# Optimization experiments

Measured on AMD Instinct MI355X. Metric: run time of the kernel, lower is better.

## Reference

```python
import jax, jax.numpy as jnp
import numpy as np

N_NODES = 100000
N_GRAPHS = 512
NEG_SLOPE = 0.2
EPS = 1e-16


def gat_conv(x, W, a_src, a_dst, bias, src, dst, heads, out_ch, concat):
    # x: [N, Fin]; W: [Fin, heads*out_ch]; a_src/a_dst: [heads, out_ch]
    N = x.shape[0]
    h = (x @ W).reshape(N, heads, out_ch)                      # [N,H,C]
    alpha_src = jnp.einsum('nhc,hc->nh', h, a_src)             # [N,H]
    alpha_dst = jnp.einsum('nhc,hc->nh', h, a_dst)             # [N,H]
    e = alpha_src[src] + alpha_dst[dst]                        # [E,H]
    e = jnp.where(e > 0, e, NEG_SLOPE * e)                     # leaky relu
    # segment softmax over incoming edges per destination node
    m = jax.ops.segment_max(e, dst, num_segments=N)            # [N,H]
    m = jnp.where(jnp.isfinite(m), m, 0.0)
    ee = jnp.exp(e - m[dst])
    denom = jax.ops.segment_sum(ee, dst, num_segments=N)       # [N,H]
    alpha = ee / (denom[dst] + EPS)                            # [E,H]
    msg = h[src] * alpha[:, :, None]                           # [E,H,C]
    out = jax.ops.segment_sum(msg, dst, num_segments=N)        # [N,H,C]
    if concat:
        out = out.reshape(N, heads * out_ch)
    else:
        out = out.mean(axis=1)
    return out + bias


def setup_inputs() -> dict:
    key = jax.random.key(0)
    ks = jax.random.split(key, 12)
    x = jax.random.normal(ks[0], (N_NODES, 128), dtype=jnp.float32)
    edge_index = jax.random.randint(ks[1], (2, 1600000), 0, N_NODES, dtype=jnp.int64)
    batch = jnp.sort(jax.random.randint(ks[2], (N_NODES,), 0, N_GRAPHS, dtype=jnp.int64))
    s = 0.1
    W1 = jax.random.normal(ks[3], (128, 64), dtype=jnp.float32) * s
    a_src1 = jax.random.normal(ks[4], (8, 8), dtype=jnp.float32) * s
    a_dst1 = jax.random.normal(ks[5], (8, 8), dtype=jnp.float32) * s
    b1 = jnp.zeros((64,), dtype=jnp.float32)
    W2 = jax.random.normal(ks[6], (64, 10), dtype=jnp.float32) * s
    a_src2 = jax.random.normal(ks[7], (1, 10), dtype=jnp.float32) * s
    a_dst2 = jax.random.normal(ks[8], (1, 10), dtype=jnp.float32) * s
    b2 = jnp.zeros((10,), dtype=jnp.float32)
    return {"x": x, "edge_index": edge_index, "batch": batch,
            "W1": W1, "a_src1": a_src1, "a_dst1": a_dst1, "b1": b1,
            "W2": W2, "a_src2": a_src2, "a_dst2": a_dst2, "b2": b2}


def reference(x, edge_index, batch, W1, a_src1, a_dst1, b1, W2, a_src2, a_dst2, b2):
    N = x.shape[0]
    # PyG GATConv default add_self_loops=True
    loops = jnp.arange(N, dtype=edge_index.dtype)
    src = jnp.concatenate([edge_index[0], loops])
    dst = jnp.concatenate([edge_index[1], loops])
    # eval mode: dropout layers are identity
    h = gat_conv(x, W1, a_src1, a_dst1, b1, src, dst, heads=8, out_ch=8, concat=True)
    h = jax.nn.elu(h)
    h = gat_conv(h, W2, a_src2, a_dst2, b2, src, dst, heads=1, out_ch=10, concat=False)
    # global mean pool over graphs
    sums = jax.ops.segment_sum(h, batch, num_segments=N_GRAPHS)        # [G,10]
    cnts = jax.ops.segment_sum(jnp.ones((N, 1), h.dtype), batch, num_segments=N_GRAPHS)
    pooled = sums / jnp.maximum(cnts, 1.0)
    return jax.nn.log_softmax(pooled, axis=1)
```

## Files before the change

kernel.cpp:

```cpp
#include <hip/hip_runtime.h>
#include <math.h>

#define L2E 1.44269504088896f
#define LRELU(v) fmaxf((v), 0.2f * (v))

__device__ __forceinline__ float fexp2(float v) { return __builtin_amdgcn_exp2f(v); }
__device__ __forceinline__ float felu(float r) {
    return r > 0.f ? r : fexp2(r * L2E) - 1.f;
}

__device__ __forceinline__ unsigned short f2bf(float f) {
    unsigned u = __float_as_uint(f);
    u += 0x7FFFu + ((u >> 16) & 1u);
    return (unsigned short)(u >> 16);
}
__device__ __forceinline__ float bf2f(unsigned short b) {
    return __uint_as_float((unsigned)b << 16);
}

typedef __attribute__((ext_vector_type(8))) short bf16x8;
typedef __attribute__((ext_vector_type(4))) float f32x4;

#define UPD8(mm, dd, Aa, Ab, ev, U)                                       \
    {                                                                     \
        float mn_ = fmaxf(mm, ev);                                        \
        float sc_ = fexp2(mm - mn_);                                      \
        float w_  = fexp2(ev - mn_);                                      \
        dd = dd * sc_ + w_;                                               \
        Aa.x = Aa.x * sc_ + w_ * __uint_as_float((U).x << 16);            \
        Aa.y = Aa.y * sc_ + w_ * __uint_as_float((U).x & 0xffff0000u);    \
        Aa.z = Aa.z * sc_ + w_ * __uint_as_float((U).y << 16);            \
        Aa.w = Aa.w * sc_ + w_ * __uint_as_float((U).y & 0xffff0000u);    \
        Ab.x = Ab.x * sc_ + w_ * __uint_as_float((U).z << 16);            \
        Ab.y = Ab.y * sc_ + w_ * __uint_as_float((U).z & 0xffff0000u);    \
        Ab.z = Ab.z * sc_ + w_ * __uint_as_float((U).w << 16);            \
        Ab.w = Ab.w * sc_ + w_ * __uint_as_float((U).w & 0xffff0000u);    \
        mm = mn_;                                                         \
    }
#define UPD1(mm, dd, aa, ev, hv)           \
    {                                      \
        float mn_ = fmaxf(mm, ev);         \
        float sc_ = fexp2(mm - mn_);       \
        float w_  = fexp2(ev - mn_);       \
        dd = dd * sc_ + w_;                \
        aa = aa * sc_ + w_ * (hv);         \
        mm = mn_;                          \
    }

#define CH 4096

__global__ __launch_bounds__(256) void k_gemm1_mfma(
        const float* __restrict__ x, const float* __restrict__ W,
        unsigned short* __restrict__ h1b, int N, int ntiles) {
    int tid = threadIdx.x;
    int w = tid >> 6, l = tid & 63;
    int c0 = w * 16;
    int lr = l & 15;
    int lg = l >> 4;

    bf16x8 bfr[4];
#pragma unroll
    for (int kk = 0; kk < 4; ++kk)
#pragma unroll
        for (int j = 0; j < 8; ++j)
            bfr[kk][j] = (short)f2bf(W[(size_t)(kk * 32 + lg * 8 + j) * 64 + c0 + lr]);

    for (int t = blockIdx.x; t < ntiles; t += gridDim.x) {
        int n0 = t * 16;
        int n = n0 + lr;
        const float4* xr = (const float4*)(x + (size_t)(n < N ? n : 0) * 128);
        f32x4 acc = {0.f, 0.f, 0.f, 0.f};
#pragma unroll
        for (int kk = 0; kk < 4; ++kk) {
            float4 u0 = xr[kk * 8 + lg * 2];
            float4 u1 = xr[kk * 8 + lg * 2 + 1];
            bf16x8 afr;
            afr[0] = (short)f2bf(u0.x); afr[1] = (short)f2bf(u0.y);
            afr[2] = (short)f2bf(u0.z); afr[3] = (short)f2bf(u0.w);
            afr[4] = (short)f2bf(u1.x); afr[5] = (short)f2bf(u1.y);
            afr[6] = (short)f2bf(u1.z); afr[7] = (short)f2bf(u1.w);
            acc = __builtin_amdgcn_mfma_f32_16x16x32_bf16(afr, bfr[kk], acc, 0, 0, 0);
        }
#pragma unroll
        for (int r = 0; r < 4; ++r) {
            int nn = n0 + lg * 4 + r;
            if (nn < N) h1b[(size_t)nn * 64 + c0 + lr] = f2bf(acc[r]);
        }
    }
}

__global__ void k_alpha(const unsigned short* __restrict__ h1b,
                        const float* __restrict__ a_src, const float* __restrict__ a_dst,
                        unsigned short* __restrict__ asrcb, float* __restrict__ adst, int N) {
    int t = blockIdx.x * 256 + threadIdx.x;
    if (t >= N * 8) return;
    int n = t >> 3, h = t & 7;
    uint4 hw = *(const uint4*)&h1b[(size_t)n * 64 + h * 8];
    const unsigned short* hu = (const unsigned short*)&hw;
    const float* as = a_src + h * 8;
    const float* ad = a_dst + h * 8;
    float s = 0.f, d = 0.f;
#pragma unroll
    for (int c = 0; c < 8; ++c) {
        float hv = bf2f(hu[c]);
        s = fmaf(hv, as[c], s);
        d = fmaf(hv, ad[c], d);
    }
    asrcb[t] = f2bf(s * L2E);
    adst[t] = d * L2E;
}


__global__ __launch_bounds__(256) void k_bhist(const int* __restrict__ dstE,
                                               const int* __restrict__ batch,
                                               int E, int NB, int G, int* __restrict__ bh) {
    __shared__ int lh[512];
    int tid = threadIdx.x, b = blockIdx.x;
    lh[tid] = 0; lh[tid + 256] = 0;
    __syncthreads();
#pragma unroll
    for (int i = 0; i < CH / 1024; ++i) {
        int eb = b * CH + (i * 256 + tid) * 4;
        if (eb + 3 < E) {
            int4 dv = *(const int4*)(dstE + eb);
            int g0 = batch[dv.x], g1 = batch[dv.y], g2 = batch[dv.z], g3 = batch[dv.w];
            atomicAdd(&lh[g0], 1); atomicAdd(&lh[g1], 1);
            atomicAdd(&lh[g2], 1); atomicAdd(&lh[g3], 1);
        } else {
#pragma unroll
            for (int k = 0; k < 4; ++k)
                if (eb + k < E) atomicAdd(&lh[batch[dstE[eb + k]]], 1);
        }
    }
    __syncthreads();
    if (tid < G)       bh[(size_t)tid * NB + b] = lh[tid];
    if (tid + 256 < G) bh[(size_t)(tid + 256) * NB + b] = lh[tid + 256];
}

__global__ __launch_bounds__(512) void k_mscan(const int* __restrict__ bh, int NB,
                                               int* __restrict__ pstart, int* __restrict__ total) {
    __shared__ int buf[512];
    int bin = blockIdx.x, t = threadIdx.x;
    int v = (t < NB) ? bh[(size_t)bin * NB + t] : 0;
    buf[t] = v;
    __syncthreads();
    for (int off = 1; off < 512; off <<= 1) {
        int u = (t >= off) ? buf[t - off] : 0;
        __syncthreads();
        buf[t] += u;
        __syncthreads();
    }
    if (t < NB) pstart[(size_t)bin * NB + t] = buf[t] - v;
    if (t == 511) total[bin] = buf[511];
}

__global__ __launch_bounds__(1024) void k_scan_top(const int* __restrict__ total, int nb,
                                                   int* __restrict__ boff,
                                                   const int* __restrict__ batch, int N,
                                                   int* __restrict__ nstart) {
    __shared__ int buf[1024];
    int t = threadIdx.x;
    int v = (t < nb) ? total[t] : 0;
    buf[t] = v;
    __syncthreads();
    for (int off = 1; off < 1024; off <<= 1) {
        int u = (t >= off) ? buf[t - off] : 0;
        __syncthreads();
        buf[t] += u;
        __syncthreads();
    }
    if (t < nb) {
        boff[t] = buf[t] - v;
        int lo = 0, hi = N;
        while (lo < hi) { int mid = (lo + hi) >> 1; if (batch[mid] < t) lo = mid + 1; else hi = mid; }
        nstart[t] = lo;
    }
}

__global__ __launch_bounds__(256) void k_bscatter(const int* __restrict__ srcE,
                                                  const int* __restrict__ dstE,
                                                  const int* __restrict__ batch,
                                                  const int* __restrict__ boff,
                                                  const int* __restrict__ pstart,
                                                  const int* __restrict__ nstart,
                                                  int E, int NB, int G, int* __restrict__ pairs) {
    __shared__ int lstart[512];
    __shared__ int lc[512];
    __shared__ int lns[512];
    int tid = threadIdx.x, b = blockIdx.x;
#pragma unroll
    for (int j = tid; j < 512; j += 256) {
        lstart[j] = (j < G) ? boff[j] + pstart[(size_t)j * NB + b] : 0;
        lns[j] = (j < G) ? nstart[j] : 0;
        lc[j] = 0;
    }
    __syncthreads();
#pragma unroll
    for (int i = 0; i < CH / 1024; ++i) {
        int eb = b * CH + (i * 256 + tid) * 4;
        if (eb + 3 < E) {
            int4 sv = *(const int4*)(srcE + eb);
            int4 dv = *(const int4*)(dstE + eb);
            int g0 = batch[dv.x], g1 = batch[dv.y], g2 = batch[dv.z], g3 = batch[dv.w];
            int p0 = atomicAdd(&lc[g0], 1);
            int p1 = atomicAdd(&lc[g1], 1);
            int p2 = atomicAdd(&lc[g2], 1);
            int p3 = atomicAdd(&lc[g3], 1);
            pairs[lstart[g0] + p0] = sv.x | ((dv.x - lns[g0]) << 17);
            pairs[lstart[g1] + p1] = sv.y | ((dv.y - lns[g1]) << 17);
            pairs[lstart[g2] + p2] = sv.z | ((dv.z - lns[g2]) << 17);
            pairs[lstart[g3] + p3] = sv.w | ((dv.w - lns[g3]) << 17);
        } else {
#pragma unroll
            for (int k = 0; k < 4; ++k)
                if (eb + k < E) {
                    int s = srcE[eb + k], d = dstE[eb + k];
                    int bin = batch[d];
                    int old = atomicAdd(&lc[bin], 1);
                    pairs[lstart[bin] + old] = s | ((d - lns[bin]) << 17);
                }
        }
    }
}

__global__ __launch_bounds__(512) void k_csr_local(const int* __restrict__ pairs,
                                                   const int* __restrict__ boff,
                                                   const int* __restrict__ batch,
                                                   int E, int N, int G,
                                                   int* __restrict__ cnt, int* __restrict__ excl,
                                                   int* __restrict__ srcs) {
    __shared__ int lcnt[512];
    __shared__ int buf[512];
    __shared__ int lcur[512];
    int g = blockIdx.x, t = threadIdx.x;
    int lo = 0, hi = N;
    while (lo < hi) { int mid = (lo + hi) >> 1; if (batch[mid] < g) lo = mid + 1; else hi = mid; }
    int ns = lo;
    hi = N;
    while (lo < hi) { int mid = (lo + hi) >> 1; if (batch[mid] < g + 1) lo = mid + 1; else hi = mid; }
    int ne = lo;
    int lnodes = ne - ns;
    int es = boff[g];
    int ee = (g + 1 < G) ? boff[g + 1] : E;

    lcnt[t] = 0;
    __syncthreads();
    for (int e = es + t; e < ee; e += 512) atomicAdd(&lcnt[pairs[e] >> 17], 1);
    __syncthreads();
    int v = lcnt[t];
    buf[t] = v;
    __syncthreads();
    for (int off = 1; off < 512; off <<= 1) {
        int u = (t >= off) ? buf[t - off] : 0;
        __syncthreads();
        buf[t] += u;
        __syncthreads();
    }
    int lex = buf[t] - v;
    lcur[t] = lex;
    if (t < lnodes) {
        cnt[ns + t] = v;
        excl[ns + t] = es + lex;
    }
    __syncthreads();
    for (int e = es + t; e < ee; e += 512) {
        int pv = pairs[e];
        int pos = atomicAdd(&lcur[pv >> 17], 1);
        srcs[es + pos] = pv & 0x1FFFF;
    }
}

__global__ void k_gather1(const int* __restrict__ srcs, const int* __restrict__ excl,
                          const int* __restrict__ cnt,
                          const unsigned short* __restrict__ asrcb, const float* __restrict__ adst1,
                          const unsigned short* __restrict__ h1b,
                          const float* __restrict__ b1, const float* __restrict__ W2,
                          const float* __restrict__ a_src2, const float* __restrict__ a_dst2,
                          unsigned short* __restrict__ h2b, unsigned short* __restrict__ asrc2b,
                          float* __restrict__ adst2, int N) {
    int tid = blockIdx.x * 256 + threadIdx.x;
    int wave = tid >> 6;
    int lane = threadIdx.x & 63;
    int q = lane >> 3;
    int l = lane & 7;
    int wid = wave * 8 + q;
    if (wid >= N) return;
    int c0 = l * 8;

    int beg = excl[wid];
    int cw  = cnt[wid];
    const int* sp = srcs + beg;
    float adh = adst1[wid * 8 + l];

    uint4 us = *(const uint4*)&h1b[(size_t)wid * 64 + c0];
    float4 A0a, A0b;
    A0a.x = __uint_as_float(us.x << 16); A0a.y = __uint_as_float(us.x & 0xffff0000u);
    A0a.z = __uint_as_float(us.y << 16); A0a.w = __uint_as_float(us.y & 0xffff0000u);
    A0b.x = __uint_as_float(us.z << 16); A0b.y = __uint_as_float(us.z & 0xffff0000u);
    A0b.z = __uint_as_float(us.w << 16); A0b.w = __uint_as_float(us.w & 0xffff0000u);
    float m0 = LRELU(bf2f(asrcb[wid * 8 + l]) + adh), d0 = 1.f;
    float4 Z = {0.f, 0.f, 0.f, 0.f};
    float4 A1a = Z, A1b = Z, A2a = Z, A2b = Z, A3a = Z, A3b = Z;
    float m1 = -INFINITY, d1 = 0.f;
    float m2 = -INFINITY, d2 = 0.f;
    float m3 = -INFINITY, d3 = 0.f;

    int i = 0;
    for (; i + 4 <= cw; i += 4) {
        int s0 = sp[i], s1 = sp[i + 1], s2 = sp[i + 2], s3 = sp[i + 3];
        float e0 = LRELU(bf2f(asrcb[s0 * 8 + l]) + adh);
        float e1 = LRELU(bf2f(asrcb[s1 * 8 + l]) + adh);
        float e2 = LRELU(bf2f(asrcb[s2 * 8 + l]) + adh);
        float e3 = LRELU(bf2f(asrcb[s3 * 8 + l]) + adh);
        uint4 u0 = *(const uint4*)&h1b[(size_t)s0 * 64 + c0];
        uint4 u1 = *(const uint4*)&h1b[(size_t)s1 * 64 + c0];
        uint4 u2 = *(const uint4*)&h1b[(size_t)s2 * 64 + c0];
        uint4 u3 = *(const uint4*)&h1b[(size_t)s3 * 64 + c0];
        UPD8(m0, d0, A0a, A0b, e0, u0);
        UPD8(m1, d1, A1a, A1b, e1, u1);
        UPD8(m2, d2, A2a, A2b, e2, u2);
        UPD8(m3, d3, A3a, A3b, e3, u3);
    }
    for (; i < cw; ++i) {
        int s = sp[i];
        float ev = LRELU(bf2f(asrcb[s * 8 + l]) + adh);
        uint4 uv = *(const uint4*)&h1b[(size_t)s * 64 + c0];
        UPD8(m0, d0, A0a, A0b, ev, uv);
    }
    float mM = fmaxf(fmaxf(m0, m1), fmaxf(m2, m3));
    float w0 = fexp2(m0 - mM), w1 = fexp2(m1 - mM);
    float w2 = fexp2(m2 - mM), w3 = fexp2(m3 - mM);
    float den = d0 * w0 + d1 * w1 + d2 * w2 + d3 * w3;
    float inv = 1.f / (den + 1e-16f);
    float rv[8];
    rv[0] = (A0a.x * w0 + A1a.x * w1 + A2a.x * w2 + A3a.x * w3) * inv;
    rv[1] = (A0a.y * w0 + A1a.y * w1 + A2a.y * w2 + A3a.y * w3) * inv;
    rv[2] = (A0a.z * w0 + A1a.z * w1 + A2a.z * w2 + A3a.z * w3) * inv;
    rv[3] = (A0a.w * w0 + A1a.w * w1 + A2a.w * w2 + A3a.w * w3) * inv;
    rv[4] = (A0b.x * w0 + A1b.x * w1 + A2b.x * w2 + A3b.x * w3) * inv;
    rv[5] = (A0b.y * w0 + A1b.y * w1 + A2b.y * w2 + A3b.y * w3) * inv;
    rv[6] = (A0b.z * w0 + A1b.z * w1 + A2b.z * w2 + A3b.z * w3) * inv;
    rv[7] = (A0b.w * w0 + A1b.w * w1 + A2b.w * w2 + A3b.w * w3) * inv;

    float accj[10];
#pragma unroll
    for (int j = 0; j < 10; ++j) accj[j] = 0.f;
#pragma unroll
    for (int t = 0; t < 8; ++t) {
        float r = felu(rv[t] + b1[c0 + t]);
        const float* wr = W2 + (c0 + t) * 10;
#pragma unroll
        for (int j = 0; j < 10; ++j) accj[j] = fmaf(r, wr[j], accj[j]);
    }
#pragma unroll
    for (int mask = 1; mask <= 4; mask <<= 1)
#pragma unroll
        for (int j = 0; j < 10; ++j) accj[j] += __shfl_xor(accj[j], mask);

    if (l == 0) {
        float s = 0.f, d = 0.f;
        unsigned pw[5];
#pragma unroll
        for (int j = 0; j < 10; j += 2) {
            s = fmaf(accj[j], a_src2[j], s);     d = fmaf(accj[j], a_dst2[j], d);
            s = fmaf(accj[j+1], a_src2[j+1], s); d = fmaf(accj[j+1], a_dst2[j+1], d);
            pw[j >> 1] = (unsigned)f2bf(accj[j]) | ((unsigned)f2bf(accj[j+1]) << 16);
        }
        unsigned* hw = (unsigned*)&h2b[(size_t)wid * 10];
#pragma unroll
        for (int j = 0; j < 5; ++j) hw[j] = pw[j];
        asrc2b[wid] = f2bf(s * L2E);
        adst2[wid] = d * L2E;
    }
}

__global__ void k_gather2(const int* __restrict__ srcs, const int* __restrict__ excl,
                          const int* __restrict__ cnt,
                          const unsigned short* __restrict__ asrc2b, const float* __restrict__ adst2,
                          const unsigned short* __restrict__ h2b, float* __restrict__ agg2, int N) {
    int tid = blockIdx.x * 256 + threadIdx.x;
    int wave = tid >> 6;
    int lane = threadIdx.x & 63;
    int q = lane >> 4;
    int l = lane & 15;
    int wid = wave * 4 + q;
    if (wid >= N) return;

    int beg = excl[wid];
    int cw  = cnt[wid];
    const int* sp = srcs + beg;
    float adn = adst2[wid];
    bool ld = l < 10;

    float m0 = LRELU(bf2f(asrc2b[wid]) + adn), d0 = 1.f;
    float a0 = ld ? bf2f(h2b[(size_t)wid * 10 + l]) : 0.f;
    float m1 = -INFINITY, d1 = 0.f, a1 = 0.f;
    float m2 = -INFINITY, d2 = 0.f, a2 = 0.f;
    float m3 = -INFINITY, d3 = 0.f, a3 = 0.f;

    int i = 0;
    for (; i + 4 <= cw; i += 4) {
        int s0 = sp[i], s1 = sp[i + 1], s2 = sp[i + 2], s3 = sp[i + 3];
        float e0 = LRELU(bf2f(asrc2b[s0]) + adn);
        float e1 = LRELU(bf2f(asrc2b[s1]) + adn);
        float e2 = LRELU(bf2f(asrc2b[s2]) + adn);
        float e3 = LRELU(bf2f(asrc2b[s3]) + adn);
        float g0 = ld ? bf2f(h2b[(size_t)s0 * 10 + l]) : 0.f;
        float g1 = ld ? bf2f(h2b[(size_t)s1 * 10 + l]) : 0.f;
        float g2 = ld ? bf2f(h2b[(size_t)s2 * 10 + l]) : 0.f;
        float g3 = ld ? bf2f(h2b[(size_t)s3 * 10 + l]) : 0.f;
        UPD1(m0, d0, a0, e0, g0);
        UPD1(m1, d1, a1, e1, g1);
        UPD1(m2, d2, a2, e2, g2);
        UPD1(m3, d3, a3, e3, g3);
    }
    for (; i < cw; ++i) {
        int s = sp[i];
        float ev = LRELU(bf2f(asrc2b[s]) + adn);
        float gv = ld ? bf2f(h2b[(size_t)s * 10 + l]) : 0.f;
        UPD1(m0, d0, a0, ev, gv);
    }
    float mM = fmaxf(fmaxf(m0, m1), fmaxf(m2, m3));
    float w0 = fexp2(m0 - mM), w1 = fexp2(m1 - mM);
    float w2 = fexp2(m2 - mM), w3 = fexp2(m3 - mM);
    float den = d0 * w0 + d1 * w1 + d2 * w2 + d3 * w3;
    float acc = a0 * w0 + a1 * w1 + a2 * w2 + a3 * w3;
    if (ld) agg2[(size_t)wid * 10 + l] = acc / (den + 1e-16f);
}

__global__ void k_pool_final(const float* __restrict__ agg2, const float* __restrict__ b2,
                             const int* __restrict__ batch, float* __restrict__ out,
                             int N, int G) {
    int g = blockIdx.x;
    int lo = 0, hi = N;
    while (lo < hi) { int mid = (lo + hi) >> 1; if (batch[mid] < g) lo = mid + 1; else hi = mid; }
    int s = lo;
    lo = s; hi = N;
    while (lo < hi) { int mid = (lo + hi) >> 1; if (batch[mid] < g + 1) lo = mid + 1; else hi = mid; }
    int e = lo;
    int tid = threadIdx.x;
    float acc[10];
#pragma unroll
    for (int j = 0; j < 10; ++j) acc[j] = 0.f;
    for (int n = s + tid; n < e; n += 256) {
        const float* r = agg2 + (size_t)n * 10;
#pragma unroll
        for (int j = 0; j < 10; ++j) acc[j] += r[j];
    }
    __shared__ float red[256 * 10];
#pragma unroll
    for (int j = 0; j < 10; ++j) red[tid * 10 + j] = acc[j];
    __syncthreads();
    for (int st = 128; st > 0; st >>= 1) {
        if (tid < st)
#pragma unroll
            for (int j = 0; j < 10; ++j) red[tid * 10 + j] += red[(tid + st) * 10 + j];
        __syncthreads();
    }
    if (tid == 0) {
        int c = e - s;
        float v[10], m = -1e30f;
#pragma unroll
        for (int j = 0; j < 10; ++j) {
            v[j] = (c > 0) ? red[j] / (float)c + b2[j] : 0.f;
            m = fmaxf(m, v[j]);
        }
        float ssum = 0.f;
#pragma unroll
        for (int j = 0; j < 10; ++j) ssum += expf(v[j] - m);
        float ls = logf(ssum);
#pragma unroll
        for (int j = 0; j < 10; ++j) out[(size_t)g * 10 + j] = v[j] - m - ls;
    }
}

extern "C" void kernel_launch(void* const* d_in, const int* in_sizes, int n_in,
                              void* d_out, int out_size, void* d_ws, size_t ws_size,
                              hipStream_t stream) {
    const float* x     = (const float*)d_in[0];
    const int*   ei    = (const int*)d_in[1];
    const int*   batch = (const int*)d_in[2];
    const float* W1    = (const float*)d_in[3];
    const float* as1w  = (const float*)d_in[4];
    const float* ad1w  = (const float*)d_in[5];
    const float* b1    = (const float*)d_in[6];
    const float* W2    = (const float*)d_in[7];
    const float* as2w  = (const float*)d_in[8];
    const float* ad2w  = (const float*)d_in[9];
    const float* b2    = (const float*)d_in[10];

    const int N  = in_sizes[0] / 128;
    const int E  = in_sizes[1] / 2;
    const int G  = out_size / 10;
    const int* srcE = ei;
    const int* dstE = ei + E;

    auto cdiv = [](long long a, long long b) { return (int)((a + b - 1) / b); };
    const int NB = cdiv(E, CH);

    size_t Nz = (size_t)N;
    unsigned short* h1b = (unsigned short*)d_ws;
    float* agg2  = (float*)d_ws;
    unsigned short* asrc1b = h1b + Nz * 64;
    float* adst1 = (float*)(asrc1b + Nz * 8);
    unsigned short* h2b = (unsigned short*)(adst1 + Nz * 8);
    unsigned short* asrc2b = h2b + Nz * 10;
    float* adst2 = (float*)(asrc2b + Nz + (Nz & 1));
    int* pairsA  = (int*)(adst2 + Nz);
    int* cntA    = pairsA + (size_t)E;
    int* exclA   = cntA + Nz;
    int* srcsA   = exclA + Nz;
    int* bhA     = srcsA + E;
    int* pstartA = bhA + (size_t)512 * NB;
    int* totalA  = pstartA + (size_t)512 * NB;
    int* boffA   = totalA + 512;
    int* nstartA = boffA + 512;

    const int B = 256;

    int ntiles = cdiv(N, 16);
    int gB = ntiles < 2048 ? ntiles : 2048;
    k_gemm1_mfma<<<gB, B, 0, stream>>>(x, W1, h1b, N, ntiles);
    k_alpha<<<cdiv((long long)N * 8, B), B, 0, stream>>>(h1b, as1w, ad1w, asrc1b, adst1, N);

    k_bhist<<<NB, B, 0, stream>>>(dstE, batch, E, NB, G, bhA);
    k_mscan<<<512, 512, 0, stream>>>(bhA, NB, pstartA, totalA);
    k_scan_top<<<1, 1024, 0, stream>>>(totalA, G, boffA, batch, N, nstartA);
    k_bscatter<<<NB, B, 0, stream>>>(srcE, dstE, batch, boffA, pstartA, nstartA, E, NB, G, pairsA);
    k_csr_local<<<G, 512, 0, stream>>>(pairsA, boffA, batch, E, N, G, cntA, exclA, srcsA);

    k_gather1<<<cdiv(N, 32), B, 0, stream>>>(srcsA, exclA, cntA, asrc1b, adst1, h1b,
                                             b1, W2, as2w, ad2w, h2b, asrc2b, adst2, N);

    k_gather2<<<cdiv(N, 16), B, 0, stream>>>(srcsA, exclA, cntA, asrc2b, adst2, h2b, agg2, N);

    k_pool_final<<<G, B, 0, stream>>>(agg2, b2, batch, (float*)d_out, N, G);
}
```

Before: 190.7 us.

## Fuse attention-logit computation into GEMM epilogue and fold top scan into mscan

```diff
diff --git a/kernel.cpp b/kernel.cpp
--- a/kernel.cpp
+++ b/kernel.cpp
@@ -51,7 +51,9 @@
 
 __global__ __launch_bounds__(256) void k_gemm1_mfma(
         const float* __restrict__ x, const float* __restrict__ W,
-        unsigned short* __restrict__ h1b, int N, int ntiles) {
+        const float* __restrict__ a_src, const float* __restrict__ a_dst,
+        unsigned short* __restrict__ h1b, unsigned short* __restrict__ asrcb,
+        float* __restrict__ adst1, int N, int ntiles) {
     int tid = threadIdx.x;
     int w = tid >> 6, l = tid & 63;
     int c0 = w * 16;
@@ -64,6 +66,9 @@
 #pragma unroll
         for (int j = 0; j < 8; ++j)
             bfr[kk][j] = (short)f2bf(W[(size_t)(kk * 32 + lg * 8 + j) * 64 + c0 + lr]);
+
+    float asv = a_src[c0 + lr];
+    float adv = a_dst[c0 + lr];
 
     for (int t = blockIdx.x; t < ntiles; t += gridDim.x) {
         int n0 = t * 16;
@@ -86,36 +91,38 @@
             int nn = n0 + lg * 4 + r;
             if (nn < N) h1b[(size_t)nn * 64 + c0 + lr] = f2bf(acc[r]);
         }
-    }
-}
-
-__global__ void k_alpha(const unsigned short* __restrict__ h1b,
-                        const float* __restrict__ a_src, const float* __restrict__ a_dst,
-                        unsigned short* __restrict__ asrcb, float* __restrict__ adst, int N) {
-    int t = blockIdx.x * 256 + threadIdx.x;
-    if (t >= N * 8) return;
-    int n = t >> 3, h = t & 7;
-    uint4 hw = *(const uint4*)&h1b[(size_t)n * 64 + h * 8];
-    const unsigned short* hu = (const unsigned short*)&hw;
-    const float* as = a_src + h * 8;
-    const float* ad = a_dst + h * 8;
-    float s = 0.f, d = 0.f;
-#pragma unroll
-    for (int c = 0; c < 8; ++c) {
-        float hv = bf2f(hu[c]);
-        s = fmaf(hv, as[c], s);
-        d = fmaf(hv, ad[c], d);
-    }
-    asrcb[t] = f2bf(s * L2E);
-    adst[t] = d * L2E;
+        float ps[4], pd[4];
+#pragma unroll
+        for (int r = 0; r < 4; ++r) { ps[r] = acc[r] * asv; pd[r] = acc[r] * adv; }
+#pragma unroll
+        for (int mask = 1; mask <= 4; mask <<= 1)
+#pragma unroll
+            for (int r = 0; r < 4; ++r) {
+                ps[r] += __shfl_xor(ps[r], mask);
+                pd[r] += __shfl_xor(pd[r], mask);
+            }
+        if ((lr & 7) == 0) {
+            int h = (c0 + lr) >> 3;
+#pragma unroll
+            for (int r = 0; r < 4; ++r) {
+                int nn = n0 + lg * 4 + r;
+                if (nn < N) {
+                    asrcb[nn * 8 + h] = f2bf(ps[r] * L2E);
+                    adst1[nn * 8 + h] = pd[r] * L2E;
+                }
+            }
+        }
+    }
 }
 
 
 __global__ __launch_bounds__(256) void k_bhist(const int* __restrict__ dstE,
                                                const int* __restrict__ batch,
-                                               int E, int NB, int G, int* __restrict__ bh) {
+                                               int E, int NB, int G, int* __restrict__ bh,
+                                               int* __restrict__ done) {
     __shared__ int lh[512];
     int tid = threadIdx.x, b = blockIdx.x;
+    if (b == 0 && tid == 0) *done = 0;
     lh[tid] = 0; lh[tid + 256] = 0;
     __syncthreads();
 #pragma unroll
@@ -138,8 +145,12 @@
 }
 
 __global__ __launch_bounds__(512) void k_mscan(const int* __restrict__ bh, int NB,
-                                               int* __restrict__ pstart, int* __restrict__ total) {
+                                               int* __restrict__ pstart, int* __restrict__ total,
+                                               int* __restrict__ boff, int* __restrict__ nstart,
+                                               const int* __restrict__ batch, int N, int G,
+                                               int* __restrict__ done) {
     __shared__ int buf[512];
+    __shared__ int isLast;
     int bin = blockIdx.x, t = threadIdx.x;
     int v = (t < NB) ? bh[(size_t)bin * NB + t] : 0;
     buf[t] = v;
@@ -152,28 +163,25 @@
     }
     if (t < NB) pstart[(size_t)bin * NB + t] = buf[t] - v;
     if (t == 511) total[bin] = buf[511];
-}
-
-__global__ __launch_bounds__(1024) void k_scan_top(const int* __restrict__ total, int nb,
-                                                   int* __restrict__ boff,
-                                                   const int* __restrict__ batch, int N,
-                                                   int* __restrict__ nstart) {
-    __shared__ int buf[1024];
-    int t = threadIdx.x;
-    int v = (t < nb) ? total[t] : 0;
-    buf[t] = v;
-    __syncthreads();
-    for (int off = 1; off < 1024; off <<= 1) {
-        int u = (t >= off) ? buf[t - off] : 0;
+    __threadfence();
+    if (t == 0) isLast = (atomicAdd(done, 1) == (int)gridDim.x - 1) ? 1 : 0;
+    __syncthreads();
+    if (isLast) {
+        int tv = (t < G) ? atomicAdd(&total[t], 0) : 0;
+        buf[t] = tv;
         __syncthreads();
-        buf[t] += u;
-        __syncthreads();
-    }
-    if (t < nb) {
-        boff[t] = buf[t] - v;
-        int lo = 0, hi = N;
-        while (lo < hi) { int mid = (lo + hi) >> 1; if (batch[mid] < t) lo = mid + 1; else hi = mid; }
-        nstart[t] = lo;
+        for (int off = 1; off < 512; off <<= 1) {
+            int u = (t >= off) ? buf[t - off] : 0;
+            __syncthreads();
+            buf[t] += u;
+            __syncthreads();
+        }
+        if (t < G) {
+            boff[t] = buf[t] - tv;
+            int lo = 0, hi = N;
+            while (lo < hi) { int mid = (lo + hi) >> 1; if (batch[mid] < t) lo = mid + 1; else hi = mid; }
+            nstart[t] = lo;
+        }
     }
 }
 
@@ -515,17 +523,16 @@
     int* totalA  = pstartA + (size_t)512 * NB;
     int* boffA   = totalA + 512;
     int* nstartA = boffA + 512;
+    int* doneA   = nstartA + 512;
 
     const int B = 256;
 
     int ntiles = cdiv(N, 16);
     int gB = ntiles < 2048 ? ntiles : 2048;
-    k_gemm1_mfma<<<gB, B, 0, stream>>>(x, W1, h1b, N, ntiles);
-    k_alpha<<<cdiv((long long)N * 8, B), B, 0, stream>>>(h1b, as1w, ad1w, asrc1b, adst1, N);
-
-    k_bhist<<<NB, B, 0, stream>>>(dstE, batch, E, NB, G, bhA);
-    k_mscan<<<512, 512, 0, stream>>>(bhA, NB, pstartA, totalA);
-    k_scan_top<<<1, 1024, 0, stream>>>(totalA, G, boffA, batch, N, nstartA);
+    k_gemm1_mfma<<<gB, B, 0, stream>>>(x, W1, as1w, ad1w, h1b, asrc1b, adst1, N, ntiles);
+
+    k_bhist<<<NB, B, 0, stream>>>(dstE, batch, E, NB, G, bhA, doneA);
+    k_mscan<<<512, 512, 0, stream>>>(bhA, NB, pstartA, totalA, boffA, nstartA, batch, N, G, doneA);
     k_bscatter<<<NB, B, 0, stream>>>(srcE, dstE, batch, boffA, pstartA, nstartA, E, NB, G, pairsA);
     k_csr_local<<<G, 512, 0, stream>>>(pairsA, boffA, batch, E, N, G, cntA, exclA, srcsA);
 
```

After: 250.5 us. +31.4%, slower.
